# Optimization experiments

Measured on AMD Instinct MI355X. Metric: run time of the kernel, lower is better.

Reference implementation:

```python
import jax, jax.numpy as jnp
import numpy as np


def setup_inputs() -> dict:
    key = jax.random.key(0)
    kq, kk, kv = jax.random.split(key, 3)
    B, S, H, HK, D = 2, 2048, 32, 8, 128
    q = jax.random.normal(kq, (B, S, H, D), dtype=jnp.float32)
    k = jax.random.normal(kk, (B, S, HK, D), dtype=jnp.float32)
    v = jax.random.normal(kv, (B, S, HK, D), dtype=jnp.float32)
    return {"q": q, "k": k, "v": v}


def reference(q, k, v):
    # Causal grouped-query attention (the math vLLM's paged attention computes
    # for a full prefill where the KV cache holds exactly this sequence).
    B, S, H, D = q.shape
    HK = k.shape[2]
    G = H // HK  # query heads per kv head
    scale = jnp.asarray(D, q.dtype) ** -0.5
    qg = q.reshape(B, S, HK, G, D)
    # scores: [B, HK, G, S(q), S(k)]
    scores = jnp.einsum("bshgd,bthd->bhgst", qg, k) * scale
    causal = jnp.tril(jnp.ones((S, S), dtype=bool))  # [Sq, Sk]
    scores = jnp.where(causal, scores, jnp.finfo(scores.dtype).min)
    probs = jax.nn.softmax(scores, axis=-1)
    out = jnp.einsum("bhgst,bthd->bshgd", probs, v)  # [B, S, HK, G, D]
    return out.reshape(B, S, H * D)
```

## Files before the change

### kernel.cpp

```cpp
#include <hip/hip_runtime.h>
#include <hip/hip_bf16.h>

typedef __attribute__((ext_vector_type(8))) short short8;
typedef __attribute__((ext_vector_type(4))) short short4v;
typedef __attribute__((ext_vector_type(4))) float f32x4;
typedef __attribute__((ext_vector_type(16))) float f32x16;

#define MFMA32(a,b,c) __builtin_amdgcn_mfma_f32_32x32x16_bf16(a,b,c,0,0,0)

static __device__ __forceinline__ short f2bf(float f){
    union{float f;unsigned u;}x; x.f=f;
    unsigned r=(x.u+0x7FFFu+((x.u>>16)&1u))>>16;
    return (short)r;
}

static __device__ __forceinline__ unsigned pkbf(float lo, float hi){
    unsigned r;
    asm("v_cvt_pk_bf16_f32 %0, %1, %2" : "=v"(r) : "v"(lo), "v"(hi));
    return r;
}

static __device__ __forceinline__ void gl_lds16(const void* g, void* l){
    __builtin_amdgcn_global_load_lds(
        (const __attribute__((address_space(1))) unsigned int*)g,
        (__attribute__((address_space(3))) unsigned int*)l, 16, 0, 0);
}

#define PACK8(s, b) ({ union{unsigned u[4]; short8 v;} w_;           \
    w_.u[0]=pkbf((s)[(b)+0],(s)[(b)+1]); w_.u[1]=pkbf((s)[(b)+2],(s)[(b)+3]); \
    w_.u[2]=pkbf((s)[(b)+4],(s)[(b)+5]); w_.u[3]=pkbf((s)[(b)+6],(s)[(b)+7]); \
    w_.v; })

constexpr int S_=2048, H_=32, HK_=8, D_=128;
constexpr int KVBLK=64;

__global__ __launch_bounds__(256) void prep(const float* __restrict__ k, const float* __restrict__ v,
                                            short* __restrict__ kb, short* __restrict__ vt){
    __shared__ short tile[64*65];
    int bid = blockIdx.x;
    if (bid < 4096){
        int t = bid*256 + threadIdx.x;
        int e = t*4;
        int d  = e & 127;
        int hk = (e>>7) & 7;
        int s  = (e>>10) & 2047;
        int b  = e>>21;
        f32x4 x = *(const f32x4*)(k + ((size_t)((b*S_+s)*HK_+hk))*D_ + d);
        short4v o;
        o[0]=f2bf(x[0]); o[1]=f2bf(x[1]); o[2]=f2bf(x[2]); o[3]=f2bf(x[3]);
        *(short4v*)(kb + ((size_t)((b*HK_+hk)*S_+s))*D_ + d) = o;
    } else {
        bid -= 4096;
        int d0 = (bid & 1)*64;
        int s0 = ((bid>>1) & 31)*64;
        int hk = (bid>>6) & 7;
        int b  = bid>>9;
        int tid = threadIdx.x;
        #pragma unroll
        for(int i=0;i<4;i++){
            int idx = i*1024 + tid*4;
            int r = idx>>6, c = idx&63;
            f32x4 x = *(const f32x4*)(v + ((size_t)((b*S_+s0+r)*HK_+hk))*D_ + d0 + c);
            tile[(c+0)*65 + r] = f2bf(x[0]);
            tile[(c+1)*65 + r] = f2bf(x[1]);
            tile[(c+2)*65 + r] = f2bf(x[2]);
            tile[(c+3)*65 + r] = f2bf(x[3]);
        }
        __syncthreads();
        #pragma unroll
        for(int i=0;i<4;i++){
            int idx = i*1024 + tid*4;
            int dr = idx>>6, c = idx&63;
            short4v o;
            o[0]=tile[dr*65+c]; o[1]=tile[dr*65+c+1]; o[2]=tile[dr*65+c+2]; o[3]=tile[dr*65+c+3];
            int m  = c & 12;
            int cp = (m==4 || m==8) ? (c ^ 12) : c;
            *(short4v*)(vt + ((size_t)((b*HK_+hk)*D_ + d0+dr))*S_ + s0 + cp) = o;
        }
    }
}

__global__ __launch_bounds__(256,2) void attn_fwd(
    const float* __restrict__ q, const short* __restrict__ kb,
    const short* __restrict__ vtb, float* __restrict__ out)
{
    __shared__ __align__(16) unsigned char kls[2][KVBLK*D_*2];
    __shared__ __align__(16) unsigned char vls[2][D_*KVBLK*2];

    const int bid  = blockIdx.x;
    const int wg   = (bid & 7)*64 + (bid >> 3);
    const int kvg  = wg >> 5;
    const int b    = kvg >> 3;
    const int hk   = kvg & 7;
    const int rr_  = wg & 31;
    const int h    = hk*4 + (rr_ >> 3);
    const int pair = rr_ & 7;

    const int tid  = threadIdx.x;
    const int wave = tid >> 6;
    const int ln   = tid & 31;
    const int hi   = (tid >> 5) & 1;

    const float qscale = 0.08838834764831845f * 1.4426950408889634f;

    const short* kt_base = kb  + (size_t)(b*HK_+hk)*S_*D_;
    const short* vt_base = vtb + (size_t)(b*HK_+hk)*D_*S_;

    auto STAGE = [&](int bufi, int kvt){
        const char* kg = (const char*)(kt_base + (size_t)kvt*KVBLK*D_);
        #pragma unroll
        for(int i=0;i<4;i++){
            int p = (i*256 + tid)*16;
            int src = p ^ (((p>>8)&7)<<4);
            gl_lds16(kg + src, &kls[bufi][p]);
        }
        const char* vg = (const char*)vt_base + (size_t)kvt*KVBLK*2;
        #pragma unroll
        for(int i=0;i<4;i++){
            int p = (i*256 + tid)*16;
            int d = p>>7;
            int src = (p&127) ^ ((d&7)<<4);
            gl_lds16(vg + (size_t)d*(S_*2) + src, &vls[bufi][p]);
        }
    };

    int cur = 0;
    STAGE(0, 0);
    __syncthreads();

    for(int phase=0; phase<2; ++phase){
        const int c      = phase ? pair : 15-pair;
        const int nkv    = 2*c + 2;
        const int kvmaxw = 2*c + (wave >> 1);
        const int qg     = c*128 + wave*32 + ln;

        short8 qf[8];
        {
            const float* qp = q + ((size_t)(b*S_ + qg)*H_ + h)*D_;
            #pragma unroll
            for(int kk=0;kk<8;kk++){
                int d0 = kk*16 + hi*8;
                f32x4 a = *(const f32x4*)(qp + d0);
                f32x4 cc= *(const f32x4*)(qp + d0 + 4);
                union{ unsigned u[4]; short8 s; } w;
                w.u[0]=pkbf(a[0]*qscale, a[1]*qscale);
                w.u[1]=pkbf(a[2]*qscale, a[3]*qscale);
                w.u[2]=pkbf(cc[0]*qscale, cc[1]*qscale);
                w.u[3]=pkbf(cc[2]*qscale, cc[3]*qscale);
                qf[kk]=w.s;
            }
        }

        f32x16 oac[4];
        #pragma unroll
        for(int dt=0;dt<4;dt++) oac[dt] = (f32x16)0.f;
        float l = 0.f;

        for(int kvt=0; kvt<nkv; ++kvt){
            int nxt = (kvt+1 < nkv) ? (kvt+1) : (phase==0 ? 0 : -1);
            if (nxt >= 0) STAGE(cur^1, nxt);

            if (kvt <= kvmaxw){
                const int kv0 = kvt*64;
                f32x16 sa0=(f32x16)0.f, sa1=(f32x16)0.f;
                const int sz = (ln&7)<<4;
                #pragma unroll
                for(int kk=0;kk<8;kk++){
                    int cb = kk*32 + hi*16;
                    short8 k0 = *(const short8*)&kls[cur][(ln*256 + cb) ^ sz];
                    short8 k1 = *(const short8*)&kls[cur][((ln+32)*256 + cb) ^ sz];
                    sa0 = MFMA32(k0, qf[kk], sa0);
                    sa1 = MFMA32(k1, qf[kk], sa1);
                }
                if (kv0 + 63 > c*128 + wave*32){
                    #pragma unroll
                    for(int r=0;r<16;r++){
                        int kvl = (r&3) + 8*(r>>2) + 4*hi;
                        if (kv0 + kvl      > qg) sa0[r] = -1e30f;
                        if (kv0 + 32 + kvl > qg) sa1[r] = -1e30f;
                    }
                }
                float ps0=0.f, ps1=0.f, ps2=0.f, ps3=0.f;
                #pragma unroll
                for(int r=0;r<16;r+=4){
                    sa0[r+0]=__builtin_amdgcn_exp2f(sa0[r+0]); ps0+=sa0[r+0];
                    sa0[r+1]=__builtin_amdgcn_exp2f(sa0[r+1]); ps1+=sa0[r+1];
                    sa0[r+2]=__builtin_amdgcn_exp2f(sa0[r+2]); ps2+=sa0[r+2];
                    sa0[r+3]=__builtin_amdgcn_exp2f(sa0[r+3]); ps3+=sa0[r+3];
                }
                #pragma unroll
                for(int r=0;r<16;r+=4){
                    sa1[r+0]=__builtin_amdgcn_exp2f(sa1[r+0]); ps0+=sa1[r+0];
                    sa1[r+1]=__builtin_amdgcn_exp2f(sa1[r+1]); ps1+=sa1[r+1];
                    sa1[r+2]=__builtin_amdgcn_exp2f(sa1[r+2]); ps2+=sa1[r+2];
                    sa1[r+3]=__builtin_amdgcn_exp2f(sa1[r+3]); ps3+=sa1[r+3];
                }
                l += (ps0+ps1)+(ps2+ps3);
                short8 pa0 = PACK8(sa0, 0);
                short8 pa1 = PACK8(sa0, 8);
                short8 pa2 = PACK8(sa1, 0);
                short8 pa3 = PACK8(sa1, 8);
                #pragma unroll
                for(int dt=0;dt<4;dt++){
                    int rb = (dt*32 + ln)*128;
                    short8 v0 = *(const short8*)&vls[cur][(rb +   0 + hi*16) ^ sz];
                    oac[dt] = MFMA32(v0, pa0, oac[dt]);
                    short8 v1 = *(const short8*)&vls[cur][(rb +  32 + hi*16) ^ sz];
                    oac[dt] = MFMA32(v1, pa1, oac[dt]);
                    short8 v2 = *(const short8*)&vls[cur][(rb +  64 + hi*16) ^ sz];
                    oac[dt] = MFMA32(v2, pa2, oac[dt]);
                    short8 v3 = *(const short8*)&vls[cur][(rb +  96 + hi*16) ^ sz];
                    oac[dt] = MFMA32(v3, pa3, oac[dt]);
                }
            }
            __syncthreads();
            cur ^= 1;
        }

        float lt = l + __shfl_xor(l, 32);
        float rinv = 1.0f / lt;
        float* op = out + ((size_t)(b*S_ + qg)*H_ + h)*D_;
        #pragma unroll
        for(int dt=0;dt<4;dt++){
            #pragma unroll
            for(int rr=0;rr<4;rr++){
                f32x4 o4;
                o4[0]=oac[dt][rr*4+0]*rinv;
                o4[1]=oac[dt][rr*4+1]*rinv;
                o4[2]=oac[dt][rr*4+2]*rinv;
                o4[3]=oac[dt][rr*4+3]*rinv;
                *(f32x4*)(op + dt*32 + rr*8 + hi*4) = o4;
            }
        }
    }
}

extern "C" void kernel_launch(void* const* d_in, const int* in_sizes, int n_in,
                              void* d_out, int out_size, void* d_ws, size_t ws_size,
                              hipStream_t stream) {
    const float* q = (const float*)d_in[0];
    const float* k = (const float*)d_in[1];
    const float* v = (const float*)d_in[2];
    float* out = (float*)d_out;

    short* kb = (short*)d_ws;
    short* vt = (short*)((char*)d_ws + (size_t)2*HK_*S_*D_*2);

    prep<<<dim3(4096+1024), dim3(256), 0, stream>>>(k, v, kb, vt);
    attn_fwd<<<dim3(512), dim3(256), 0, stream>>>(q, kb, vt, out);
}
```

Measured before the change: 103.8 us.

## Software-pipeline QK and softmax-PV over 32-row KV tiles with 4-slot LDS ring

Splits each 64-row KV block into 32-row tiles held in a four-buffer LDS ring, and software-pipelines the loop so the QK^T MFMA for the next tile is issued alongside the exp/softmax and PV MFMAs of the current one. The finer tiles also let each wave stop at its own diagonal tile, so causal masking only applies to a single tile per wave. The goal is to overlap matrix-core work with the exp and pack VALU work. In exchange there are twice as many barriers per KV row, more live registers for the second score accumulator, and the cross-phase prefetch is dropped in favour of a re-prologue at each phase.

```diff
diff --git a/kernel.cpp b/kernel.cpp
--- a/kernel.cpp
+++ b/kernel.cpp
@@ -32,7 +32,6 @@
     w_.v; })
 
 constexpr int S_=2048, H_=32, HK_=8, D_=128;
-constexpr int KVBLK=64;
 
 __global__ __launch_bounds__(256) void prep(const float* __restrict__ k, const float* __restrict__ v,
                                             short* __restrict__ kb, short* __restrict__ vt){
@@ -84,8 +83,8 @@
     const float* __restrict__ q, const short* __restrict__ kb,
     const short* __restrict__ vtb, float* __restrict__ out)
 {
-    __shared__ __align__(16) unsigned char kls[2][KVBLK*D_*2];
-    __shared__ __align__(16) unsigned char vls[2][D_*KVBLK*2];
+    __shared__ __align__(16) unsigned char kls[4][32*256];
+    __shared__ __align__(16) unsigned char vls[4][128*64];
 
     const int bid  = blockIdx.x;
     const int wg   = (bid & 7)*64 + (bid >> 3);
@@ -106,32 +105,29 @@
     const short* kt_base = kb  + (size_t)(b*HK_+hk)*S_*D_;
     const short* vt_base = vtb + (size_t)(b*HK_+hk)*D_*S_;
 
-    auto STAGE = [&](int bufi, int kvt){
-        const char* kg = (const char*)(kt_base + (size_t)kvt*KVBLK*D_);
-        #pragma unroll
-        for(int i=0;i<4;i++){
+    auto STAGE = [&](int t){
+        const int bi = t & 3;
+        const char* kg = (const char*)(kt_base + (size_t)t*32*D_);
+        #pragma unroll
+        for(int i=0;i<2;i++){
             int p = (i*256 + tid)*16;
             int src = p ^ (((p>>8)&7)<<4);
-            gl_lds16(kg + src, &kls[bufi][p]);
-        }
-        const char* vg = (const char*)vt_base + (size_t)kvt*KVBLK*2;
-        #pragma unroll
-        for(int i=0;i<4;i++){
+            gl_lds16(kg + src, &kls[bi][p]);
+        }
+        const char* vg = (const char*)vt_base + (size_t)t*32*2;
+        #pragma unroll
+        for(int i=0;i<2;i++){
             int p = (i*256 + tid)*16;
-            int d = p>>7;
-            int src = (p&127) ^ ((d&7)<<4);
-            gl_lds16(vg + (size_t)d*(S_*2) + src, &vls[bufi][p]);
+            int d = p>>6;
+            int src = (p&63) ^ ((d&3)<<4);
+            gl_lds16(vg + (size_t)d*(S_*2) + src, &vls[bi][p]);
         }
     };
-
-    int cur = 0;
-    STAGE(0, 0);
-    __syncthreads();
 
     for(int phase=0; phase<2; ++phase){
         const int c      = phase ? pair : 15-pair;
-        const int nkv    = 2*c + 2;
-        const int kvmaxw = 2*c + (wave >> 1);
+        const int ntiles = 4*c + 4;
+        const int wl     = 4*c + wave;
         const int qg     = c*128 + wave*32 + ln;
 
         short8 qf[8];
@@ -156,65 +152,64 @@
         for(int dt=0;dt<4;dt++) oac[dt] = (f32x16)0.f;
         float l = 0.f;
 
-        for(int kvt=0; kvt<nkv; ++kvt){
-            int nxt = (kvt+1 < nkv) ? (kvt+1) : (phase==0 ? 0 : -1);
-            if (nxt >= 0) STAGE(cur^1, nxt);
-
-            if (kvt <= kvmaxw){
-                const int kv0 = kvt*64;
-                f32x16 sa0=(f32x16)0.f, sa1=(f32x16)0.f;
-                const int sz = (ln&7)<<4;
+        const int sz = (ln&7)<<4;
+        const int vsz = (ln&3)<<4;
+
+        auto QK = [&](int tt, f32x16 &sa){
+            const int bi = tt & 3;
+            sa = (f32x16)0.f;
+            #pragma unroll
+            for(int kk=0;kk<8;kk++){
+                short8 k0 = *(const short8*)&kls[bi][(ln*256 + kk*32 + hi*16) ^ sz];
+                sa = MFMA32(k0, qf[kk], sa);
+            }
+            if (tt == wl){
                 #pragma unroll
-                for(int kk=0;kk<8;kk++){
-                    int cb = kk*32 + hi*16;
-                    short8 k0 = *(const short8*)&kls[cur][(ln*256 + cb) ^ sz];
-                    short8 k1 = *(const short8*)&kls[cur][((ln+32)*256 + cb) ^ sz];
-                    sa0 = MFMA32(k0, qf[kk], sa0);
-                    sa1 = MFMA32(k1, qf[kk], sa1);
+                for(int r=0;r<16;r++){
+                    int kvl = (r&3) + 8*(r>>2) + 4*hi;
+                    if (kvl > ln) sa[r] = -1e30f;
                 }
-                if (kv0 + 63 > c*128 + wave*32){
-                    #pragma unroll
-                    for(int r=0;r<16;r++){
-                        int kvl = (r&3) + 8*(r>>2) + 4*hi;
-                        if (kv0 + kvl      > qg) sa0[r] = -1e30f;
-                        if (kv0 + 32 + kvl > qg) sa1[r] = -1e30f;
-                    }
-                }
-                float ps0=0.f, ps1=0.f, ps2=0.f, ps3=0.f;
-                #pragma unroll
-                for(int r=0;r<16;r+=4){
-                    sa0[r+0]=__builtin_amdgcn_exp2f(sa0[r+0]); ps0+=sa0[r+0];
-                    sa0[r+1]=__builtin_amdgcn_exp2f(sa0[r+1]); ps1+=sa0[r+1];
-                    sa0[r+2]=__builtin_amdgcn_exp2f(sa0[r+2]); ps2+=sa0[r+2];
-                    sa0[r+3]=__builtin_amdgcn_exp2f(sa0[r+3]); ps3+=sa0[r+3];
-                }
-                #pragma unroll
-                for(int r=0;r<16;r+=4){
-                    sa1[r+0]=__builtin_amdgcn_exp2f(sa1[r+0]); ps0+=sa1[r+0];
-                    sa1[r+1]=__builtin_amdgcn_exp2f(sa1[r+1]); ps1+=sa1[r+1];
-                    sa1[r+2]=__builtin_amdgcn_exp2f(sa1[r+2]); ps2+=sa1[r+2];
-                    sa1[r+3]=__builtin_amdgcn_exp2f(sa1[r+3]); ps3+=sa1[r+3];
-                }
-                l += (ps0+ps1)+(ps2+ps3);
-                short8 pa0 = PACK8(sa0, 0);
-                short8 pa1 = PACK8(sa0, 8);
-                short8 pa2 = PACK8(sa1, 0);
-                short8 pa3 = PACK8(sa1, 8);
-                #pragma unroll
-                for(int dt=0;dt<4;dt++){
-                    int rb = (dt*32 + ln)*128;
-                    short8 v0 = *(const short8*)&vls[cur][(rb +   0 + hi*16) ^ sz];
-                    oac[dt] = MFMA32(v0, pa0, oac[dt]);
-                    short8 v1 = *(const short8*)&vls[cur][(rb +  32 + hi*16) ^ sz];
-                    oac[dt] = MFMA32(v1, pa1, oac[dt]);
-                    short8 v2 = *(const short8*)&vls[cur][(rb +  64 + hi*16) ^ sz];
-                    oac[dt] = MFMA32(v2, pa2, oac[dt]);
-                    short8 v3 = *(const short8*)&vls[cur][(rb +  96 + hi*16) ^ sz];
-                    oac[dt] = MFMA32(v3, pa3, oac[dt]);
-                }
-            }
+            }
+        };
+
+        auto SMPV = [&](int tt, f32x16 &sa){
+            const int bi = tt & 3;
+            float ps0=0.f, ps1=0.f, ps2=0.f, ps3=0.f;
+            #pragma unroll
+            for(int r=0;r<16;r+=4){
+                sa[r+0]=__builtin_amdgcn_exp2f(sa[r+0]); ps0+=sa[r+0];
+                sa[r+1]=__builtin_amdgcn_exp2f(sa[r+1]); ps1+=sa[r+1];
+                sa[r+2]=__builtin_amdgcn_exp2f(sa[r+2]); ps2+=sa[r+2];
+                sa[r+3]=__builtin_amdgcn_exp2f(sa[r+3]); ps3+=sa[r+3];
+            }
+            l += (ps0+ps1)+(ps2+ps3);
+            short8 pa0 = PACK8(sa, 0);
+            short8 pa1 = PACK8(sa, 8);
+            #pragma unroll
+            for(int dt=0;dt<4;dt++){
+                int rb = (dt*32 + ln)*64;
+                short8 v0 = *(const short8*)&vls[bi][(rb +  0 + hi*16) ^ vsz];
+                oac[dt] = MFMA32(v0, pa0, oac[dt]);
+                short8 v1 = *(const short8*)&vls[bi][(rb + 32 + hi*16) ^ vsz];
+                oac[dt] = MFMA32(v1, pa1, oac[dt]);
+            }
+        };
+
+        f32x16 saA, saB;
+
+        STAGE(0); STAGE(1);
+        __syncthreads();
+        QK(0, saA);
+
+        for(int t=0; t<ntiles; t+=2){
+            if (t+2 < ntiles) STAGE(t+2);
+            if (t+1 <= wl) QK(t+1, saB);
+            if (t   <= wl) SMPV(t, saA);
             __syncthreads();
-            cur ^= 1;
+            if (t+3 < ntiles) STAGE(t+3);
+            if (t+2 < ntiles && t+2 <= wl) QK(t+2, saA);
+            if (t+1 <= wl) SMPV(t+1, saB);
+            __syncthreads();
         }
 
         float lt = l + __shfl_xor(l, 32);
@@ -232,6 +227,7 @@
                 *(f32x4*)(op + dt*32 + rr*8 + hi*4) = o4;
             }
         }
+        __syncthreads();
     }
 }
 
```

After: 112.6 us. +8.6%, slower.

## Split paired causal tiles into separate blocks and drop LDS double buffering

Applied to the files above, without the earlier changes.

Each workgroup now handles one 128-row query chunk instead of a balanced pair, so the grid doubles to 1024 blocks. Blocks are ordered longest-first with an XCD-aware mapping so each XCD shares a KV head. LDS double buffering is removed, which halves shared memory, and launch bounds are raised to allow 3 blocks per CU. In exchange, loads are no longer overlapped with compute, since each KV tile is staged and synchronized before use, and load balance now relies on the hardware scheduler.

```diff
diff --git a/kernel.cpp b/kernel.cpp
--- a/kernel.cpp
+++ b/kernel.cpp
@@ -80,157 +80,157 @@
     }
 }
 
-__global__ __launch_bounds__(256,2) void attn_fwd(
+__global__ __launch_bounds__(256,3) void attn_fwd(
     const float* __restrict__ q, const short* __restrict__ kb,
     const short* __restrict__ vtb, float* __restrict__ out)
 {
-    __shared__ __align__(16) unsigned char kls[2][KVBLK*D_*2];
-    __shared__ __align__(16) unsigned char vls[2][D_*KVBLK*2];
+    __shared__ __align__(16) unsigned char kls[KVBLK*D_*2];
+    __shared__ __align__(16) unsigned char vls[D_*KVBLK*2];
 
     const int bid  = blockIdx.x;
-    const int wg   = (bid & 7)*64 + (bid >> 3);
-    const int kvg  = wg >> 5;
+    const int s    = bid >> 8;
+    const int j    = bid & 255;
+    const int xcd  = j & 7;
+    const int t    = j >> 3;
+    const int kvg  = xcd*2 + (t & 1);
+    const int u    = t >> 1;
+    const int hsub = u & 3;
+    const int cq   = u >> 2;
+    int c;
+    switch(s){ case 0: c = 15-cq; break; case 1: c = 8+cq; break;
+               case 2: c = 7-cq;  break; default: c = cq; }
     const int b    = kvg >> 3;
     const int hk   = kvg & 7;
-    const int rr_  = wg & 31;
-    const int h    = hk*4 + (rr_ >> 3);
-    const int pair = rr_ & 7;
+    const int h    = hk*4 + hsub;
+    const int q0   = c * 128;
 
     const int tid  = threadIdx.x;
     const int wave = tid >> 6;
     const int ln   = tid & 31;
     const int hi   = (tid >> 5) & 1;
+    const int qg   = q0 + wave*32 + ln;
 
     const float qscale = 0.08838834764831845f * 1.4426950408889634f;
 
     const short* kt_base = kb  + (size_t)(b*HK_+hk)*S_*D_;
     const short* vt_base = vtb + (size_t)(b*HK_+hk)*D_*S_;
 
-    auto STAGE = [&](int bufi, int kvt){
+    short8 qf[8];
+    {
+        const float* qp = q + ((size_t)(b*S_ + qg)*H_ + h)*D_;
+        #pragma unroll
+        for(int kk=0;kk<8;kk++){
+            int d0 = kk*16 + hi*8;
+            f32x4 a = *(const f32x4*)(qp + d0);
+            f32x4 cc= *(const f32x4*)(qp + d0 + 4);
+            union{ unsigned u[4]; short8 s; } w;
+            w.u[0]=pkbf(a[0]*qscale, a[1]*qscale);
+            w.u[1]=pkbf(a[2]*qscale, a[3]*qscale);
+            w.u[2]=pkbf(cc[0]*qscale, cc[1]*qscale);
+            w.u[3]=pkbf(cc[2]*qscale, cc[3]*qscale);
+            qf[kk]=w.s;
+        }
+    }
+
+    f32x16 oac[4];
+    #pragma unroll
+    for(int dt=0;dt<4;dt++) oac[dt] = (f32x16)0.f;
+    float l = 0.f;
+
+    auto STAGE = [&](int kvt){
         const char* kg = (const char*)(kt_base + (size_t)kvt*KVBLK*D_);
         #pragma unroll
         for(int i=0;i<4;i++){
-            int p = (i*256 + tid)*16;
-            int src = p ^ (((p>>8)&7)<<4);
-            gl_lds16(kg + src, &kls[bufi][p]);
+            int pp = (i*256 + tid)*16;
+            int src = pp ^ (((pp>>8)&7)<<4);
+            gl_lds16(kg + src, &kls[pp]);
         }
         const char* vg = (const char*)vt_base + (size_t)kvt*KVBLK*2;
         #pragma unroll
         for(int i=0;i<4;i++){
-            int p = (i*256 + tid)*16;
-            int d = p>>7;
-            int src = (p&127) ^ ((d&7)<<4);
-            gl_lds16(vg + (size_t)d*(S_*2) + src, &vls[bufi][p]);
+            int pp = (i*256 + tid)*16;
+            int d = pp>>7;
+            int src = (pp&127) ^ ((d&7)<<4);
+            gl_lds16(vg + (size_t)d*(S_*2) + src, &vls[pp]);
         }
     };
 
-    int cur = 0;
-    STAGE(0, 0);
-    __syncthreads();
-
-    for(int phase=0; phase<2; ++phase){
-        const int c      = phase ? pair : 15-pair;
-        const int nkv    = 2*c + 2;
-        const int kvmaxw = 2*c + (wave >> 1);
-        const int qg     = c*128 + wave*32 + ln;
-
-        short8 qf[8];
-        {
-            const float* qp = q + ((size_t)(b*S_ + qg)*H_ + h)*D_;
+    const int nkv    = 2*c + 2;
+    const int kvmaxw = 2*c + (wave >> 1);
+
+    for(int kvt=0; kvt<nkv; ++kvt){
+        if (kvt) __syncthreads();
+        STAGE(kvt);
+        __syncthreads();
+
+        if (kvt <= kvmaxw){
+            const int kv0 = kvt*64;
+            const int sz = (ln&7)<<4;
+            f32x16 sa0=(f32x16)0.f, sa1=(f32x16)0.f;
             #pragma unroll
             for(int kk=0;kk<8;kk++){
-                int d0 = kk*16 + hi*8;
-                f32x4 a = *(const f32x4*)(qp + d0);
-                f32x4 cc= *(const f32x4*)(qp + d0 + 4);
-                union{ unsigned u[4]; short8 s; } w;
-                w.u[0]=pkbf(a[0]*qscale, a[1]*qscale);
-                w.u[1]=pkbf(a[2]*qscale, a[3]*qscale);
-                w.u[2]=pkbf(cc[0]*qscale, cc[1]*qscale);
-                w.u[3]=pkbf(cc[2]*qscale, cc[3]*qscale);
-                qf[kk]=w.s;
-            }
-        }
-
-        f32x16 oac[4];
-        #pragma unroll
-        for(int dt=0;dt<4;dt++) oac[dt] = (f32x16)0.f;
-        float l = 0.f;
-
-        for(int kvt=0; kvt<nkv; ++kvt){
-            int nxt = (kvt+1 < nkv) ? (kvt+1) : (phase==0 ? 0 : -1);
-            if (nxt >= 0) STAGE(cur^1, nxt);
-
-            if (kvt <= kvmaxw){
-                const int kv0 = kvt*64;
-                f32x16 sa0=(f32x16)0.f, sa1=(f32x16)0.f;
-                const int sz = (ln&7)<<4;
+                int cb = kk*32 + hi*16;
+                short8 k0 = *(const short8*)&kls[(ln*256 + cb) ^ sz];
+                short8 k1 = *(const short8*)&kls[((ln+32)*256 + cb) ^ sz];
+                sa0 = MFMA32(k0, qf[kk], sa0);
+                sa1 = MFMA32(k1, qf[kk], sa1);
+            }
+            if (kv0 + 63 > q0 + wave*32){
                 #pragma unroll
-                for(int kk=0;kk<8;kk++){
-                    int cb = kk*32 + hi*16;
-                    short8 k0 = *(const short8*)&kls[cur][(ln*256 + cb) ^ sz];
-                    short8 k1 = *(const short8*)&kls[cur][((ln+32)*256 + cb) ^ sz];
-                    sa0 = MFMA32(k0, qf[kk], sa0);
-                    sa1 = MFMA32(k1, qf[kk], sa1);
+                for(int r=0;r<16;r++){
+                    int kvl = (r&3) + 8*(r>>2) + 4*hi;
+                    if (kv0 + kvl      > qg) sa0[r] = -1e30f;
+                    if (kv0 + 32 + kvl > qg) sa1[r] = -1e30f;
                 }
-                if (kv0 + 63 > c*128 + wave*32){
-                    #pragma unroll
-                    for(int r=0;r<16;r++){
-                        int kvl = (r&3) + 8*(r>>2) + 4*hi;
-                        if (kv0 + kvl      > qg) sa0[r] = -1e30f;
-                        if (kv0 + 32 + kvl > qg) sa1[r] = -1e30f;
-                    }
-                }
-                float ps0=0.f, ps1=0.f, ps2=0.f, ps3=0.f;
-                #pragma unroll
-                for(int r=0;r<16;r+=4){
-                    sa0[r+0]=__builtin_amdgcn_exp2f(sa0[r+0]); ps0+=sa0[r+0];
-                    sa0[r+1]=__builtin_amdgcn_exp2f(sa0[r+1]); ps1+=sa0[r+1];
-                    sa0[r+2]=__builtin_amdgcn_exp2f(sa0[r+2]); ps2+=sa0[r+2];
-                    sa0[r+3]=__builtin_amdgcn_exp2f(sa0[r+3]); ps3+=sa0[r+3];
-                }
-                #pragma unroll
-                for(int r=0;r<16;r+=4){
-                    sa1[r+0]=__builtin_amdgcn_exp2f(sa1[r+0]); ps0+=sa1[r+0];
-                    sa1[r+1]=__builtin_amdgcn_exp2f(sa1[r+1]); ps1+=sa1[r+1];
-                    sa1[r+2]=__builtin_amdgcn_exp2f(sa1[r+2]); ps2+=sa1[r+2];
-                    sa1[r+3]=__builtin_amdgcn_exp2f(sa1[r+3]); ps3+=sa1[r+3];
-                }
-                l += (ps0+ps1)+(ps2+ps3);
-                short8 pa0 = PACK8(sa0, 0);
-                short8 pa1 = PACK8(sa0, 8);
-                short8 pa2 = PACK8(sa1, 0);
-                short8 pa3 = PACK8(sa1, 8);
-                #pragma unroll
-                for(int dt=0;dt<4;dt++){
-                    int rb = (dt*32 + ln)*128;
-                    short8 v0 = *(const short8*)&vls[cur][(rb +   0 + hi*16) ^ sz];
-                    oac[dt] = MFMA32(v0, pa0, oac[dt]);
-                    short8 v1 = *(const short8*)&vls[cur][(rb +  32 + hi*16) ^ sz];
-                    oac[dt] = MFMA32(v1, pa1, oac[dt]);
-                    short8 v2 = *(const short8*)&vls[cur][(rb +  64 + hi*16) ^ sz];
-                    oac[dt] = MFMA32(v2, pa2, oac[dt]);
-                    short8 v3 = *(const short8*)&vls[cur][(rb +  96 + hi*16) ^ sz];
-                    oac[dt] = MFMA32(v3, pa3, oac[dt]);
-                }
-            }
-            __syncthreads();
-            cur ^= 1;
-        }
-
-        float lt = l + __shfl_xor(l, 32);
-        float rinv = 1.0f / lt;
-        float* op = out + ((size_t)(b*S_ + qg)*H_ + h)*D_;
-        #pragma unroll
-        for(int dt=0;dt<4;dt++){
-            #pragma unroll
-            for(int rr=0;rr<4;rr++){
-                f32x4 o4;
-                o4[0]=oac[dt][rr*4+0]*rinv;
-                o4[1]=oac[dt][rr*4+1]*rinv;
-                o4[2]=oac[dt][rr*4+2]*rinv;
-                o4[3]=oac[dt][rr*4+3]*rinv;
-                *(f32x4*)(op + dt*32 + rr*8 + hi*4) = o4;
-            }
+            }
+            float ps0=0.f, ps1=0.f, ps2=0.f, ps3=0.f;
+            #pragma unroll
+            for(int r=0;r<16;r+=4){
+                sa0[r+0]=__builtin_amdgcn_exp2f(sa0[r+0]); ps0+=sa0[r+0];
+                sa0[r+1]=__builtin_amdgcn_exp2f(sa0[r+1]); ps1+=sa0[r+1];
+                sa0[r+2]=__builtin_amdgcn_exp2f(sa0[r+2]); ps2+=sa0[r+2];
+                sa0[r+3]=__builtin_amdgcn_exp2f(sa0[r+3]); ps3+=sa0[r+3];
+            }
+            #pragma unroll
+            for(int r=0;r<16;r+=4){
+                sa1[r+0]=__builtin_amdgcn_exp2f(sa1[r+0]); ps0+=sa1[r+0];
+                sa1[r+1]=__builtin_amdgcn_exp2f(sa1[r+1]); ps1+=sa1[r+1];
+                sa1[r+2]=__builtin_amdgcn_exp2f(sa1[r+2]); ps2+=sa1[r+2];
+                sa1[r+3]=__builtin_amdgcn_exp2f(sa1[r+3]); ps3+=sa1[r+3];
+            }
+            l += (ps0+ps1)+(ps2+ps3);
+            short8 pa0 = PACK8(sa0, 0);
+            short8 pa1 = PACK8(sa0, 8);
+            short8 pa2 = PACK8(sa1, 0);
+            short8 pa3 = PACK8(sa1, 8);
+            #pragma unroll
+            for(int dt=0;dt<4;dt++){
+                int rb = (dt*32 + ln)*128;
+                short8 v0 = *(const short8*)&vls[(rb +   0 + hi*16) ^ sz];
+                oac[dt] = MFMA32(v0, pa0, oac[dt]);
+                short8 v1 = *(const short8*)&vls[(rb +  32 + hi*16) ^ sz];
+                oac[dt] = MFMA32(v1, pa1, oac[dt]);
+                short8 v2 = *(const short8*)&vls[(rb +  64 + hi*16) ^ sz];
+                oac[dt] = MFMA32(v2, pa2, oac[dt]);
+                short8 v3 = *(const short8*)&vls[(rb +  96 + hi*16) ^ sz];
+                oac[dt] = MFMA32(v3, pa3, oac[dt]);
+            }
+        }
+    }
+
+    float lt = l + __shfl_xor(l, 32);
+    float rinv = 1.0f / lt;
+    float* op = out + ((size_t)(b*S_ + qg)*H_ + h)*D_;
+    #pragma unroll
+    for(int dt=0;dt<4;dt++){
+        #pragma unroll
+        for(int rr=0;rr<4;rr++){
+            f32x4 o4;
+            o4[0]=oac[dt][rr*4+0]*rinv;
+            o4[1]=oac[dt][rr*4+1]*rinv;
+            o4[2]=oac[dt][rr*4+2]*rinv;
+            o4[3]=oac[dt][rr*4+3]*rinv;
+            *(f32x4*)(op + dt*32 + rr*8 + hi*4) = o4;
         }
     }
 }
@@ -247,5 +247,5 @@
     short* vt = (short*)((char*)d_ws + (size_t)2*HK_*S_*D_*2);
 
     prep<<<dim3(4096+1024), dim3(256), 0, stream>>>(k, v, kb, vt);
-    attn_fwd<<<dim3(512), dim3(256), 0, stream>>>(q, kb, vt, out);
-}
+    attn_fwd<<<dim3(1024), dim3(256), 0, stream>>>(q, kb, vt, out);
+}
```

Result: slower. 168.6 us (+62.5%).
